# Optimization experiments

Measured on AMD Instinct MI355X. Metric: run time of the kernel, lower is better.

The kernel has to match this reference:

```python
import jax, jax.numpy as jnp
import numpy as np

B, N, CPTS = 16, 4096, 64
M, K, RADIUS = 1024, 32, 0.2
MLP = [64, 64, 128]
EPS = 1e-5  # torch BatchNorm2d default


def setup_inputs() -> dict:
    key = jax.random.key(0)
    ks = jax.random.split(key, 2 + len(MLP))
    inp = {
        "xyz": jax.random.uniform(ks[0], (B, N, 3), dtype=jnp.float32),
        "points": jax.random.normal(ks[1], (B, N, CPTS), dtype=jnp.float32),
    }
    cin = 3 + CPTS
    for i, cout in enumerate(MLP):
        inp[f"W{i}"] = jax.random.normal(ks[2 + i], (cout, cin), dtype=jnp.float32) / np.sqrt(cin)
        inp[f"g{i}"] = jnp.ones((cout,), jnp.float32)
        inp[f"b{i}"] = jnp.zeros((cout,), jnp.float32)
        cin = cout
    return inp


def fps(xyz, m):
    # Farthest point sampling, deterministic start at index 0. Returns (B, m) int32.
    b, n, _ = xyz.shape

    def step(carry, _):
        min_d, far = carry
        cent = jnp.take_along_axis(xyz, far[:, None, None], axis=1)  # (B,1,3)
        d = jnp.sum((xyz - cent) ** 2, axis=-1)                      # (B,N)
        min_d = jnp.minimum(min_d, d)
        return (min_d, jnp.argmax(min_d, axis=-1).astype(jnp.int32)), far

    init = (jnp.full((b, n), 1e10, xyz.dtype), jnp.zeros((b,), jnp.int32))
    _, inds = jax.lax.scan(step, init, None, length=m)
    return inds.T  # (B, m)


def ball_query(xyz, new_xyz, radius, k):
    # Euclidean distances (B,M,N); indices within radius, first-k, pad with first valid.
    d2 = (jnp.sum(new_xyz ** 2, -1)[:, :, None] + jnp.sum(xyz ** 2, -1)[:, None, :]
          - 2.0 * jnp.einsum('bmc,bnc->bmn', new_xyz, xyz))
    dists = jnp.sqrt(jnp.maximum(d2, 0.0))
    n = xyz.shape[1]
    idx = jnp.where(dists > radius, n, jnp.arange(n, dtype=jnp.int32)[None, None, :])
    idx = jnp.sort(idx, axis=-1)[:, :, :k]          # first k in-radius indices (N-padded)
    first = idx[:, :, :1]                           # centroid itself (dist 0) always valid
    return jnp.where(idx == n, first, idx)          # (B, M, k)


def reference(xyz, points, W0, g0, b0, W1, g1, b1, W2, g2, b2):
    bidx = jnp.arange(B)[:, None]
    fps_inds = fps(xyz, M)                          # (B, M)
    new_xyz = xyz[bidx, fps_inds]                   # (B, M, 3)
    g_inds = ball_query(xyz, new_xyz, RADIUS, K)    # (B, M, K)
    bidx2 = jnp.arange(B)[:, None, None]
    grouped_xyz = xyz[bidx2, g_inds] - new_xyz[:, :, None, :]   # (B,M,K,3) local coords
    grouped_pts = points[bidx2, g_inds]                          # (B,M,K,C)
    feats = jnp.concatenate([grouped_xyz, grouped_pts], axis=-1)  # (B,M,K,3+C)

    # 1x1 Conv2d (no bias) + BatchNorm2d (training-mode batch stats) + ReLU
    for Wi, gi, bi in ((W0, g0, b0), (W1, g1, b1), (W2, g2, b2)):
        h = jnp.einsum('bmkc,oc->bmko', feats, Wi)
        mean = h.mean(axis=(0, 1, 2))
        var = h.var(axis=(0, 1, 2))
        feats = jax.nn.relu(gi * (h - mean) * jax.lax.rsqrt(var + EPS) + bi)

    new_points = feats.max(axis=2)                  # max-pool over K -> (B, M, 128)
    return new_xyz, new_points, g_inds
```

## Files before the change

kernel.cpp:

```cpp
#include <hip/hip_runtime.h>
#include <hip/hip_bf16.h>
#include <cstdint>

#define B_ 16
#define N_ 4096
#define CPTS_ 64
#define M_ 1024
#define K_ 32
#define MF_TOT 2097152

using ushort8 = __attribute__((ext_vector_type(8))) unsigned short;
using bf16x8  = __attribute__((ext_vector_type(8))) short;
using f32x4v  = __attribute__((ext_vector_type(4))) float;

static __device__ __forceinline__ unsigned f2bf(float x){
  unsigned u = __float_as_uint(x);
  return (u + 0x7fffu + ((u >> 16) & 1u)) >> 16;
}
static __device__ __forceinline__ float bf2f(unsigned short u){
  return __uint_as_float(((unsigned)u) << 16);
}

#define DPPMAX(v, ctrl)                                                        \
  do {                                                                         \
    int _t = __builtin_amdgcn_update_dpp(0, __float_as_int(v), (ctrl), 0xf,    \
                                         0xf, true);                           \
    (v) = fmaxf((v), __int_as_float(_t));                                      \
  } while (0)

#define STEP(MD, PX, PY, PZ, C, J)                                             \
  { float dx = PX.C - cx, dy = PY.C - cy, dz = PZ.C - cz;                      \
    float d = dx * dx; d = d + dy * dy; d = d + dz * dz;                       \
    float nm = fminf(MD.C, d); MD.C = nm;                                      \
    if (nm > bv){ bv = nm; bj = (J); } }
#define STEP4(MD, PX, PY, PZ, J0)                                              \
  STEP(MD, PX, PY, PZ, x, J0)                                                  \
  STEP(MD, PX, PY, PZ, y, (J0) + 1)                                            \
  STEP(MD, PX, PY, PZ, z, (J0) + 2)                                            \
  STEP(MD, PX, PY, PZ, w, (J0) + 3)

__global__ __launch_bounds__(512, 1) void fps_kernel(const float* __restrict__ xyz,
                                                     float* __restrict__ newxyz){
#pragma clang fp contract(off)
  __shared__ float xs[N_], ys[N_], zs[N_];
  __shared__ int inds_s[M_];
  __shared__ unsigned long long sv_[2][8];
  const int b = blockIdx.x, tid = threadIdx.x;
  const int lane = tid & 63, wv = tid >> 6;
  const float* xb = xyz + (size_t)b * N_ * 3;
  for (int i = tid; i < N_ * 3; i += 512){
    float v = xb[i];
    int n = i / 3, c = i - n * 3;
    if (c == 0) xs[n] = v; else if (c == 1) ys[n] = v; else zs[n] = v;
  }
  __syncthreads();
  const float4 px0 = *reinterpret_cast<const float4*>(&xs[tid * 8 + 0]);
  const float4 px1 = *reinterpret_cast<const float4*>(&xs[tid * 8 + 4]);
  const float4 py0 = *reinterpret_cast<const float4*>(&ys[tid * 8 + 0]);
  const float4 py1 = *reinterpret_cast<const float4*>(&ys[tid * 8 + 4]);
  const float4 pz0 = *reinterpret_cast<const float4*>(&zs[tid * 8 + 0]);
  const float4 pz1 = *reinterpret_cast<const float4*>(&zs[tid * 8 + 4]);
  float4 md0 = make_float4(1e10f, 1e10f, 1e10f, 1e10f);
  float4 md1 = md0;
  int far = 0;
  float cx = xs[0], cy = ys[0], cz = zs[0];
  for (int m = 0; m < M_; ++m){
    if (tid == 0) inds_s[m] = far;
    float bv = -1.0f; int bj = 0;
    STEP4(md0, px0, py0, pz0, 0)
    STEP4(md1, px1, py1, pz1, 4)
    float wm = bv;
    DPPMAX(wm, 0x111);
    DPPMAX(wm, 0x112);
    DPPMAX(wm, 0x114);
    DPPMAX(wm, 0x118);
    DPPMAX(wm, 0x142);
    DPPMAX(wm, 0x143);
    const float wmax = __int_as_float(
        __builtin_amdgcn_readlane(__float_as_int(wm), 63));
    unsigned long long tied = __ballot(bv == wmax);
    const int winlane = (int)__builtin_ctzll(tied);
    const int sl = m & 1;
    if (lane == winlane){
      int wn = tid * 8 + bj;
      sv_[sl][wv] = ((unsigned long long)__float_as_uint(wmax) << 32)
                  | (unsigned)(4095 - wn);
    }
    __syncthreads();
    unsigned long long p0 = sv_[sl][0], p1 = sv_[sl][1], p2 = sv_[sl][2], p3 = sv_[sl][3];
    unsigned long long p4 = sv_[sl][4], p5 = sv_[sl][5], p6 = sv_[sl][6], p7 = sv_[sl][7];
    if (p1 > p0) p0 = p1;
    if (p3 > p2) p2 = p3;
    if (p5 > p4) p4 = p5;
    if (p7 > p6) p6 = p7;
    if (p2 > p0) p0 = p2;
    if (p6 > p4) p4 = p6;
    if (p4 > p0) p0 = p4;
    far = 4095 - (int)(p0 & 0xffffffffu);
    cx = xs[far]; cy = ys[far]; cz = zs[far];
  }
  __syncthreads();
  for (int t = tid; t < M_; t += 512){
    int id = inds_s[t];
    size_t o = ((size_t)b * M_ + t) * 3;
    newxyz[o] = xs[id]; newxyz[o + 1] = ys[id]; newxyz[o + 2] = zs[id];
  }
}

__global__ __launch_bounds__(256) void phi_kernel(const float* __restrict__ xyz,
                                                  const float* __restrict__ points,
                                                  const float* __restrict__ W,
                                                  float* __restrict__ phi){
  __shared__ __align__(16) float Wt[67][64];
  __shared__ __align__(16) float ft[67][128];
  const int tid = threadIdx.x, blk = blockIdx.x;
  const int p0 = blk * 128;
  for (int i = tid; i < 67 * 64; i += 256){
    int o = i / 67, c = i - o * 67;
    Wt[c][o] = W[i];
  }
  const int sl = tid >> 1, half = tid & 1;
  const int p = p0 + sl;
  const float* ps = points + (size_t)p * CPTS_ + half * 32;
  #pragma unroll
  for (int j = 0; j < 8; ++j){
    float4 v = *reinterpret_cast<const float4*>(ps + j * 4);
    int c = 3 + half * 32 + j * 4;
    ft[c][sl] = v.x; ft[c + 1][sl] = v.y; ft[c + 2][sl] = v.z; ft[c + 3][sl] = v.w;
  }
  if (half == 0){
    const float* xp = xyz + (size_t)p * 3;
    ft[0][sl] = xp[0]; ft[1][sl] = xp[1]; ft[2][sl] = xp[2];
  }
  __syncthreads();
  const int sg = tid & 31, og = tid >> 5;
  float acc[4][8];
  #pragma unroll
  for (int i = 0; i < 4; ++i)
    #pragma unroll
    for (int o = 0; o < 8; ++o) acc[i][o] = 0.0f;
  #pragma unroll 2
  for (int c = 0; c < 67; ++c){
    float4 f = *reinterpret_cast<const float4*>(&ft[c][sg * 4]);
    float4 w0 = *reinterpret_cast<const float4*>(&Wt[c][og * 8]);
    float4 w1 = *reinterpret_cast<const float4*>(&Wt[c][og * 8 + 4]);
    const float fv[4] = {f.x, f.y, f.z, f.w};
    #pragma unroll
    for (int i = 0; i < 4; ++i){
      acc[i][0] += fv[i] * w0.x; acc[i][1] += fv[i] * w0.y;
      acc[i][2] += fv[i] * w0.z; acc[i][3] += fv[i] * w0.w;
      acc[i][4] += fv[i] * w1.x; acc[i][5] += fv[i] * w1.y;
      acc[i][6] += fv[i] * w1.z; acc[i][7] += fv[i] * w1.w;
    }
  }
  #pragma unroll
  for (int i = 0; i < 4; ++i){
    float* dst = phi + (size_t)(p0 + sg * 4 + i) * 64 + og * 8;
    *reinterpret_cast<float4*>(dst)     = make_float4(acc[i][0], acc[i][1], acc[i][2], acc[i][3]);
    *reinterpret_cast<float4*>(dst + 4) = make_float4(acc[i][4], acc[i][5], acc[i][6], acc[i][7]);
  }
}

__global__ __launch_bounds__(256) void ballq_psi_kernel(const float* __restrict__ xyz,
                                                        const float* __restrict__ newxyz,
                                                        int* __restrict__ gi,
                                                        float* __restrict__ gif,
                                                        const float* __restrict__ W0,
                                                        float* __restrict__ psi){
  if (blockIdx.x >= 4096){
    const int mi = (blockIdx.x - 4096) * 256 + threadIdx.x;
    const float x = newxyz[(size_t)mi * 3];
    const float y = newxyz[(size_t)mi * 3 + 1];
    const float z = newxyz[(size_t)mi * 3 + 2];
    float* dst = psi + (size_t)mi * 64;
    #pragma unroll
    for (int o4 = 0; o4 < 16; ++o4){
      float v[4];
      #pragma unroll
      for (int e = 0; e < 4; ++e){
        int o = o4 * 4 + e;
        v[e] = fmaf(z, W0[o * 67 + 2], fmaf(y, W0[o * 67 + 1], x * W0[o * 67]));
      }
      *reinterpret_cast<float4*>(dst + o4 * 4) = make_float4(v[0], v[1], v[2], v[3]);
    }
    return;
  }
  const int gw = (blockIdx.x * 256 + threadIdx.x) >> 6;
  const int lane = threadIdx.x & 63;
  const int b = gw >> 10, m = gw & 1023;
  const float* xb = xyz + (size_t)b * N_ * 3;
  const size_t no = (size_t)b * M_ + m;
  const float cx = newxyz[no * 3], cy = newxyz[no * 3 + 1], cz = newxyz[no * 3 + 2];
  const float sm = fmaf(cz, cz, fmaf(cy, cy, cx * cx));
  int total = 0, first_idx = 0; bool havef = false;
  int*   gd = gi  + no * K_;
  float* fd = gif + no * K_;
  for (int ch = 0; ch < 64 && total < K_; ++ch){
    const int n = ch * 64 + lane;
    const float x = xb[n * 3], y = xb[n * 3 + 1], z = xb[n * 3 + 2];
    const float sn = fmaf(z, z, fmaf(y, y, x * x));
    const float dt = fmaf(z, cz, fmaf(y, cy, x * cx));
    float d2 = (sm + sn) - 2.0f * dt;
    float dist = sqrtf(fmaxf(d2, 0.0f));
    bool pred = !(dist > 0.2f);
    unsigned long long mask = __ballot(pred);
    if (!havef && mask){ havef = true; first_idx = ch * 64 + (int)__builtin_ctzll(mask); }
    if (pred){
      int rank = total + (int)__popcll(mask & ((1ull << lane) - 1ull));
      if (rank < K_){ gd[rank] = n; fd[rank] = (float)n; }
    }
    total += (int)__popcll(mask);
  }
  if (total < K_ && lane >= total && lane < K_){ gd[lane] = first_idx; fd[lane] = (float)first_idx; }
}

__global__ __launch_bounds__(256) void stats0_kernel(const float* __restrict__ phi,
                                                     const float* __restrict__ psi,
                                                     const int* __restrict__ gi,
                                                     float* __restrict__ part){
  __shared__ int gidx[128];
  __shared__ float psm[4][64];
  const int tid = threadIdx.x, blk = blockIdx.x;
  const size_t s0 = (size_t)blk * 128;
  const int b  = (int)(s0 >> 15);
  const int m0 = ((int)(s0 & 32767)) >> 5;
  if (tid < 128) gidx[tid] = gi[(size_t)b * 32768 + (size_t)m0 * K_ + tid];
  psm[tid >> 6][tid & 63] =
      psi[((size_t)b * M_ + m0 + (tid >> 6)) * 64 + (tid & 63)];
  __syncthreads();
  const int sg = tid & 31, og = tid >> 5;
  const int mi = sg >> 3;
  float sv[8], sq[8];
  #pragma unroll
  for (int o = 0; o < 8; ++o){ sv[o] = 0.f; sq[o] = 0.f; }
  #pragma unroll
  for (int i = 0; i < 4; ++i){
    const int g = gidx[sg * 4 + i];
    const float* gp = phi + ((size_t)b * N_ + g) * 64 + og * 8;
    float4 a0 = *reinterpret_cast<const float4*>(gp);
    float4 a1 = *reinterpret_cast<const float4*>(gp + 4);
    const float pv[8] = {a0.x, a0.y, a0.z, a0.w, a1.x, a1.y, a1.z, a1.w};
    #pragma unroll
    for (int o = 0; o < 8; ++o){
      float v = pv[o] - psm[mi][og * 8 + o];
      sv[o] += v; sq[o] += v * v;
    }
  }
  #pragma unroll
  for (int off = 1; off < 32; off <<= 1){
    #pragma unroll
    for (int o = 0; o < 8; ++o){
      sv[o] += __shfl_xor(sv[o], off);
      sq[o] += __shfl_xor(sq[o], off);
    }
  }
  if (sg == 0){
    #pragma unroll
    for (int o = 0; o < 8; ++o){
      int ch = og * 8 + o;
      part[(size_t)(ch * 2) * 4096 + blk]     = sv[o];
      part[(size_t)(ch * 2 + 1) * 4096 + blk] = sq[o];
    }
  }
}

template<int CIN, int COUT>
__global__ __launch_bounds__(256) void mlp1_pass(
    const float* __restrict__ phi, const float* __restrict__ psi,
    const int* __restrict__ gi, const float* __restrict__ bnin,
    const float* __restrict__ W,
    unsigned short* __restrict__ hout, float* __restrict__ part)
{
  constexpr int OPT = COUT / 8;
  __shared__ __align__(16) float Wt[CIN][COUT];
  __shared__ __align__(16) float ft[CIN][128];
  const int tid = threadIdx.x, blk = blockIdx.x;
  const size_t s0 = (size_t)blk * 128;

  for (int i = tid; i < CIN * COUT; i += 256){
    int o = i / CIN, c = i - o * CIN;
    Wt[c][o] = W[i];
  }
  {
    __shared__ int gidx[128];
    __shared__ float psm[4][64];
    const int b  = (int)(s0 >> 15);
    const int m0 = ((int)(s0 & 32767)) >> 5;
    if (tid < 128) gidx[tid] = gi[(size_t)b * 32768 + (size_t)m0 * K_ + tid];
    psm[tid >> 6][tid & 63] =
        psi[((size_t)b * M_ + m0 + (tid >> 6)) * 64 + (tid & 63)];
    __syncthreads();
    const int sl = tid >> 1, half = tid & 1;
    const int g = gidx[sl];
    const int mi = sl >> 5;
    const float* gp = phi + ((size_t)b * N_ + g) * 64 + half * 32;
    #pragma unroll
    for (int j = 0; j < 8; ++j){
      float4 v = *reinterpret_cast<const float4*>(gp + j * 4);
      int c = half * 32 + j * 4;
      ft[c][sl]     = fmaxf((v.x - psm[mi][c])     * bnin[c]     + bnin[CIN + c],     0.0f);
      ft[c + 1][sl] = fmaxf((v.y - psm[mi][c + 1]) * bnin[c + 1] + bnin[CIN + c + 1], 0.0f);
      ft[c + 2][sl] = fmaxf((v.z - psm[mi][c + 2]) * bnin[c + 2] + bnin[CIN + c + 2], 0.0f);
      ft[c + 3][sl] = fmaxf((v.w - psm[mi][c + 3]) * bnin[c + 3] + bnin[CIN + c + 3], 0.0f);
    }
  }
  __syncthreads();

  const int sg = tid & 31, og = tid >> 5;
  float acc[4][OPT];
  #pragma unroll
  for (int i = 0; i < 4; ++i)
    #pragma unroll
    for (int o = 0; o < OPT; ++o) acc[i][o] = 0.0f;

  #pragma unroll 2
  for (int c = 0; c < CIN; ++c){
    float4 f = *reinterpret_cast<const float4*>(&ft[c][sg * 4]);
    float4 w[OPT / 4];
    #pragma unroll
    for (int j = 0; j < OPT / 4; ++j)
      w[j] = *reinterpret_cast<const float4*>(&Wt[c][og * OPT + j * 4]);
    const float fv[4] = {f.x, f.y, f.z, f.w};
    #pragma unroll
    for (int i = 0; i < 4; ++i){
      #pragma unroll
      for (int j = 0; j < OPT / 4; ++j){
        acc[i][j * 4 + 0] += fv[i] * w[j].x;
        acc[i][j * 4 + 1] += fv[i] * w[j].y;
        acc[i][j * 4 + 2] += fv[i] * w[j].z;
        acc[i][j * 4 + 3] += fv[i] * w[j].w;
      }
    }
  }

  #pragma unroll
  for (int i = 0; i < 4; ++i){
    size_t s = s0 + sg * 4 + i;
    unsigned pk[OPT / 2];
    #pragma unroll
    for (int o = 0; o < OPT / 2; ++o)
      pk[o] = f2bf(acc[i][2 * o]) | (f2bf(acc[i][2 * o + 1]) << 16);
    uint4* dst = reinterpret_cast<uint4*>(hout + s * COUT + og * OPT);
    dst[0] = make_uint4(pk[0], pk[1], pk[2], pk[3]);
  }
  float sv[OPT], sq[OPT];
  #pragma unroll
  for (int o = 0; o < OPT; ++o){
    float a0 = acc[0][o], a1 = acc[1][o], a2 = acc[2][o], a3 = acc[3][o];
    sv[o] = ((a0 + a1) + a2) + a3;
    sq[o] = ((a0 * a0 + a1 * a1) + a2 * a2) + a3 * a3;
  }
  #pragma unroll
  for (int off = 1; off < 32; off <<= 1){
    #pragma unroll
    for (int o = 0; o < OPT; ++o){
      sv[o] += __shfl_xor(sv[o], off);
      sq[o] += __shfl_xor(sq[o], off);
    }
  }
  if (sg == 0){
    #pragma unroll
    for (int o = 0; o < OPT; ++o){
      int ch = og * OPT + o;
      part[(size_t)(ch * 2) * 4096 + blk]     = sv[o];
      part[(size_t)(ch * 2 + 1) * 4096 + blk] = sq[o];
    }
  }
}

__global__ __launch_bounds__(256) void mlp2_mfma(
    const unsigned short* __restrict__ h1, const float* __restrict__ bn1,
    const float* __restrict__ W2, float* __restrict__ part,
    float* __restrict__ mxmn)
{
  __shared__ unsigned short wsh[128 * 72], wsl[128 * 72];
  __shared__ unsigned short fsh[128 * 72], fsl[128 * 72];
  const int tid = threadIdx.x, blk = blockIdx.x;
  const size_t s0 = (size_t)blk * 128;

  for (int i = tid; i < 128 * 64; i += 256){
    int o = i >> 6, c = i & 63;
    float f = W2[i];
    unsigned hb = f2bf(f);
    float res = f - bf2f((unsigned short)hb);
    wsh[o * 72 + c] = (unsigned short)hb;
    wsl[o * 72 + c] = (unsigned short)f2bf(res);
  }
  {
    const int sl = tid >> 1, c0 = (tid & 1) * 32;
    const unsigned short* hp = h1 + (s0 + sl) * 64 + c0;
    #pragma unroll
    for (int j = 0; j < 4; ++j){
      ushort8 raw = *reinterpret_cast<const ushort8*>(hp + j * 8);
      ushort8 ph, pl;
      #pragma unroll
      for (int e = 0; e < 8; ++e){
        int c = c0 + j * 8 + e;
        float f = fmaxf(bf2f(raw[e]) * bn1[c] + bn1[64 + c], 0.0f);
        unsigned hb = f2bf(f);
        float res = f - bf2f((unsigned short)hb);
        ph[e] = (unsigned short)hb;
        pl[e] = (unsigned short)f2bf(res);
      }
      *reinterpret_cast<ushort8*>(&fsh[sl * 72 + c0 + j * 8]) = ph;
      *reinterpret_cast<ushort8*>(&fsl[sl * 72 + c0 + j * 8]) = pl;
    }
  }
  __syncthreads();

  const int l = tid & 63, w = tid >> 6;
  const int col = l & 15, g = l >> 4;

  bf16x8 bh[2][2], bl[2][2];
  #pragma unroll
  for (int ot = 0; ot < 2; ++ot)
    #pragma unroll
    for (int ks = 0; ks < 2; ++ks){
      int a = (w * 32 + ot * 16 + col) * 72 + ks * 32 + g * 8;
      bh[ot][ks] = *reinterpret_cast<const bf16x8*>(&wsh[a]);
      bl[ot][ks] = *reinterpret_cast<const bf16x8*>(&wsl[a]);
    }

  f32x4v acc[8][2];
  #pragma unroll
  for (int st = 0; st < 8; ++st)
    #pragma unroll
    for (int ot = 0; ot < 2; ++ot)
      acc[st][ot] = (f32x4v){0.f, 0.f, 0.f, 0.f};

  #pragma unroll
  for (int st = 0; st < 8; ++st){
    bf16x8 ah[2], al[2];
    #pragma unroll
    for (int ks = 0; ks < 2; ++ks){
      int a = (st * 16 + col) * 72 + ks * 32 + g * 8;
      ah[ks] = *reinterpret_cast<const bf16x8*>(&fsh[a]);
      al[ks] = *reinterpret_cast<const bf16x8*>(&fsl[a]);
    }
    #pragma unroll
    for (int ot = 0; ot < 2; ++ot){
      #pragma unroll
      for (int ks = 0; ks < 2; ++ks){
        acc[st][ot] = __builtin_amdgcn_mfma_f32_16x16x32_bf16(ah[ks], bh[ot][ks], acc[st][ot], 0, 0, 0);
        acc[st][ot] = __builtin_amdgcn_mfma_f32_16x16x32_bf16(ah[ks], bl[ot][ks], acc[st][ot], 0, 0, 0);
        acc[st][ot] = __builtin_amdgcn_mfma_f32_16x16x32_bf16(al[ks], bh[ot][ks], acc[st][ot], 0, 0, 0);
      }
    }
  }

  #pragma unroll
  for (int ot = 0; ot < 2; ++ot){
    const int ch = w * 32 + ot * 16 + col;
    float sv = 0.f, sq = 0.f;
    float mxm[4], mnm[4];
    #pragma unroll
    for (int j = 0; j < 4; ++j){ mxm[j] = -1e30f; mnm[j] = 1e30f; }
    #pragma unroll
    for (int st = 0; st < 8; ++st){
      f32x4v a = acc[st][ot];
      float t0 = a[0], t1 = a[1], t2 = a[2], t3 = a[3];
      sv += ((t0 + t1) + t2) + t3;
      sq += ((t0 * t0 + t1 * t1) + t2 * t2) + t3 * t3;
      float tmx = fmaxf(fmaxf(t0, t1), fmaxf(t2, t3));
      float tmn = fminf(fminf(t0, t1), fminf(t2, t3));
      mxm[st >> 1] = fmaxf(mxm[st >> 1], tmx);
      mnm[st >> 1] = fminf(mnm[st >> 1], tmn);
    }
    sv += __shfl_xor(sv, 16); sv += __shfl_xor(sv, 32);
    sq += __shfl_xor(sq, 16); sq += __shfl_xor(sq, 32);
    #pragma unroll
    for (int j = 0; j < 4; ++j){
      mxm[j] = fmaxf(mxm[j], __shfl_xor(mxm[j], 16));
      mxm[j] = fmaxf(mxm[j], __shfl_xor(mxm[j], 32));
      mnm[j] = fminf(mnm[j], __shfl_xor(mnm[j], 16));
      mnm[j] = fminf(mnm[j], __shfl_xor(mnm[j], 32));
    }
    if (g == 0){
      part[(size_t)(ch * 2) * 4096 + blk]     = sv;
      part[(size_t)(ch * 2 + 1) * 4096 + blk] = sq;
      #pragma unroll
      for (int j = 0; j < 4; ++j){
        size_t mf = (s0 >> 5) + j;
        mxmn[mf * 128 + ch]          = mxm[j];
        mxmn[MF_TOT + mf * 128 + ch] = mnm[j];
      }
    }
  }
}

__global__ __launch_bounds__(256) void reduce_stats(const float* __restrict__ part,
                                                    const float* __restrict__ g,
                                                    const float* __restrict__ bb,
                                                    float* __restrict__ bn, int cout){
  const int ch = blockIdx.x, tid = threadIdx.x;
  float s = 0.f, q = 0.f;
  const float* ps = part + (size_t)(ch * 2) * 4096;
  const float* pq = part + (size_t)(ch * 2 + 1) * 4096;
  for (int i = tid; i < 4096; i += 256){ s += ps[i]; q += pq[i]; }
  #pragma unroll
  for (int off = 1; off < 64; off <<= 1){ s += __shfl_xor(s, off); q += __shfl_xor(q, off); }
  __shared__ float as_[4], aq_[4];
  if ((tid & 63) == 0){ as_[tid >> 6] = s; aq_[tid >> 6] = q; }
  __syncthreads();
  if (tid == 0){
    float S = as_[0] + as_[1] + as_[2] + as_[3];
    float Q = aq_[0] + aq_[1] + aq_[2] + aq_[3];
    const float cnt = 524288.0f;
    float mean = S / cnt;
    float var  = Q / cnt - mean * mean;
    float sc = g[ch] / sqrtf(var + 1e-5f);
    bn[ch] = sc;
    bn[cout + ch] = bb[ch] - mean * sc;
  }
}

__global__ __launch_bounds__(256) void bn_minmax_finish(const float* __restrict__ mxmn,
                                                        const float* __restrict__ bn2,
                                                        float* __restrict__ out){
  const int i = blockIdx.x * 256 + threadIdx.x;
  const int ch = i & 127;
  const float a = bn2[ch], sh = bn2[128 + ch];
  const float mx = mxmn[i], mn = mxmn[MF_TOT + i];
  out[i] = fmaxf(fmaxf(mx * a + sh, mn * a + sh), 0.0f);
}

extern "C" void kernel_launch(void* const* d_in, const int* in_sizes, int n_in,
                              void* d_out, int out_size, void* d_ws, size_t ws_size,
                              hipStream_t stream){
  (void)in_sizes; (void)n_in; (void)out_size; (void)ws_size;
  const float* xyz    = (const float*)d_in[0];
  const float* points = (const float*)d_in[1];
  const float* W0 = (const float*)d_in[2];
  const float* g0 = (const float*)d_in[3];
  const float* b0 = (const float*)d_in[4];
  const float* W1 = (const float*)d_in[5];
  const float* g1 = (const float*)d_in[6];
  const float* b1 = (const float*)d_in[7];
  const float* W2 = (const float*)d_in[8];
  const float* g2 = (const float*)d_in[9];
  const float* b2 = (const float*)d_in[10];

  float* out = (float*)d_out;
  float* o_newxyz = out;
  float* o_newpts = out + (size_t)B_ * M_ * 3;
  float* o_gind   = out + (size_t)B_ * M_ * 3 + (size_t)B_ * M_ * 128;

  char* ws = (char*)d_ws;
  int*   gi   = (int*)(ws + 0);
  float* part = (float*)(ws + (2ull << 20));
  float* bn0  = (float*)(ws + (6ull << 20));
  float* bn1  = (float*)(ws + (6ull << 20) + 1024);
  float* bn2  = (float*)(ws + (6ull << 20) + 2048);
  float* phi  = (float*)(ws + (8ull << 20));
  float* psi  = (float*)(ws + (24ull << 20));
  unsigned short* h1 = (unsigned short*)(ws + (28ull << 20));
  float* mxmn = (float*)(ws + (92ull << 20));

  phi_kernel<<<512, 256, 0, stream>>>(xyz, points, W0, phi);
  fps_kernel<<<16, 512, 0, stream>>>(xyz, o_newxyz);
  ballq_psi_kernel<<<4160, 256, 0, stream>>>(xyz, o_newxyz, gi, o_gind, W0, psi);

  stats0_kernel<<<4096, 256, 0, stream>>>(phi, psi, gi, part);
  reduce_stats<<<64, 256, 0, stream>>>(part, g0, b0, bn0, 64);

  mlp1_pass<64, 64><<<4096, 256, 0, stream>>>(phi, psi, gi, bn0, W1, h1, part);
  reduce_stats<<<64, 256, 0, stream>>>(part, g1, b1, bn1, 64);

  mlp2_mfma<<<4096, 256, 0, stream>>>(h1, bn1, W2, part, mxmn);
  reduce_stats<<<128, 256, 0, stream>>>(part, g2, b2, bn2, 128);
  bn_minmax_finish<<<MF_TOT / 256, 256, 0, stream>>>(mxmn, bn2, o_newpts);
}
```

Baseline: 938.0 us.

## Replace scalar FP32 layer-1 GEMM with split-bf16 MFMA kernel

Replaces the templated scalar FMA kernel for the second 1x1 conv layer with an MFMA version, mirroring the existing layer-2 kernel. Weights and gathered, normalized activations are split into bf16 hi/lo pairs in shared memory, and three 16x16x32 bf16 MFMAs per k-step approximate an FP32 product. The goal is to cut the ALU cost of the 64x64 GEMM over 524K samples. In exchange it adds split/convert work, scattered 2-byte output stores instead of 16-byte vector stores, and a small precision change from the three-term bf16 split.

```diff
diff --git a/kernel.cpp b/kernel.cpp
--- a/kernel.cpp
+++ b/kernel.cpp
@@ -264,107 +264,109 @@
   }
 }
 
-template<int CIN, int COUT>
-__global__ __launch_bounds__(256) void mlp1_pass(
+__global__ __launch_bounds__(256) void mlp1_mfma(
     const float* __restrict__ phi, const float* __restrict__ psi,
-    const int* __restrict__ gi, const float* __restrict__ bnin,
-    const float* __restrict__ W,
-    unsigned short* __restrict__ hout, float* __restrict__ part)
+    const int* __restrict__ gi, const float* __restrict__ bn0,
+    const float* __restrict__ W1,
+    unsigned short* __restrict__ h1, float* __restrict__ part)
 {
-  constexpr int OPT = COUT / 8;
-  __shared__ __align__(16) float Wt[CIN][COUT];
-  __shared__ __align__(16) float ft[CIN][128];
+  __shared__ unsigned short wsh[64 * 72], wsl[64 * 72];
+  __shared__ unsigned short fsh[128 * 72], fsl[128 * 72];
+  __shared__ int gidx[128];
+  __shared__ float psm[4][64];
   const int tid = threadIdx.x, blk = blockIdx.x;
   const size_t s0 = (size_t)blk * 128;
-
-  for (int i = tid; i < CIN * COUT; i += 256){
-    int o = i / CIN, c = i - o * CIN;
-    Wt[c][o] = W[i];
-  }
+  const int b  = (int)(s0 >> 15);
+  const int m0 = ((int)(s0 & 32767)) >> 5;
+
+  for (int i = tid; i < 64 * 64; i += 256){
+    int o = i >> 6, c = i & 63;
+    float f = W1[i];
+    unsigned hb = f2bf(f);
+    float res = f - bf2f((unsigned short)hb);
+    wsh[o * 72 + c] = (unsigned short)hb;
+    wsl[o * 72 + c] = (unsigned short)f2bf(res);
+  }
+  if (tid < 128) gidx[tid] = gi[(size_t)b * 32768 + (size_t)m0 * K_ + tid];
+  psm[tid >> 6][tid & 63] =
+      psi[((size_t)b * M_ + m0 + (tid >> 6)) * 64 + (tid & 63)];
+  __syncthreads();
   {
-    __shared__ int gidx[128];
-    __shared__ float psm[4][64];
-    const int b  = (int)(s0 >> 15);
-    const int m0 = ((int)(s0 & 32767)) >> 5;
-    if (tid < 128) gidx[tid] = gi[(size_t)b * 32768 + (size_t)m0 * K_ + tid];
-    psm[tid >> 6][tid & 63] =
-        psi[((size_t)b * M_ + m0 + (tid >> 6)) * 64 + (tid & 63)];
-    __syncthreads();
     const int sl = tid >> 1, half = tid & 1;
     const int g = gidx[sl];
     const int mi = sl >> 5;
     const float* gp = phi + ((size_t)b * N_ + g) * 64 + half * 32;
     #pragma unroll
-    for (int j = 0; j < 8; ++j){
-      float4 v = *reinterpret_cast<const float4*>(gp + j * 4);
-      int c = half * 32 + j * 4;
-      ft[c][sl]     = fmaxf((v.x - psm[mi][c])     * bnin[c]     + bnin[CIN + c],     0.0f);
-      ft[c + 1][sl] = fmaxf((v.y - psm[mi][c + 1]) * bnin[c + 1] + bnin[CIN + c + 1], 0.0f);
-      ft[c + 2][sl] = fmaxf((v.z - psm[mi][c + 2]) * bnin[c + 2] + bnin[CIN + c + 2], 0.0f);
-      ft[c + 3][sl] = fmaxf((v.w - psm[mi][c + 3]) * bnin[c + 3] + bnin[CIN + c + 3], 0.0f);
-    }
-  }
-  __syncthreads();
-
-  const int sg = tid & 31, og = tid >> 5;
-  float acc[4][OPT];
-  #pragma unroll
-  for (int i = 0; i < 4; ++i)
-    #pragma unroll
-    for (int o = 0; o < OPT; ++o) acc[i][o] = 0.0f;
-
-  #pragma unroll 2
-  for (int c = 0; c < CIN; ++c){
-    float4 f = *reinterpret_cast<const float4*>(&ft[c][sg * 4]);
-    float4 w[OPT / 4];
-    #pragma unroll
-    for (int j = 0; j < OPT / 4; ++j)
-      w[j] = *reinterpret_cast<const float4*>(&Wt[c][og * OPT + j * 4]);
-    const float fv[4] = {f.x, f.y, f.z, f.w};
-    #pragma unroll
-    for (int i = 0; i < 4; ++i){
+    for (int jj = 0; jj < 4; ++jj){
+      float4 v0 = *reinterpret_cast<const float4*>(gp + jj * 8);
+      float4 v1 = *reinterpret_cast<const float4*>(gp + jj * 8 + 4);
+      const float vv[8] = {v0.x, v0.y, v0.z, v0.w, v1.x, v1.y, v1.z, v1.w};
+      ushort8 ph, pl;
       #pragma unroll
-      for (int j = 0; j < OPT / 4; ++j){
-        acc[i][j * 4 + 0] += fv[i] * w[j].x;
-        acc[i][j * 4 + 1] += fv[i] * w[j].y;
-        acc[i][j * 4 + 2] += fv[i] * w[j].z;
-        acc[i][j * 4 + 3] += fv[i] * w[j].w;
+      for (int e = 0; e < 8; ++e){
+        int c = half * 32 + jj * 8 + e;
+        float f = fmaxf((vv[e] - psm[mi][c]) * bn0[c] + bn0[64 + c], 0.0f);
+        unsigned hb = f2bf(f);
+        float res = f - bf2f((unsigned short)hb);
+        ph[e] = (unsigned short)hb;
+        pl[e] = (unsigned short)f2bf(res);
       }
-    }
-  }
-
-  #pragma unroll
-  for (int i = 0; i < 4; ++i){
-    size_t s = s0 + sg * 4 + i;
-    unsigned pk[OPT / 2];
-    #pragma unroll
-    for (int o = 0; o < OPT / 2; ++o)
-      pk[o] = f2bf(acc[i][2 * o]) | (f2bf(acc[i][2 * o + 1]) << 16);
-    uint4* dst = reinterpret_cast<uint4*>(hout + s * COUT + og * OPT);
-    dst[0] = make_uint4(pk[0], pk[1], pk[2], pk[3]);
-  }
-  float sv[OPT], sq[OPT];
-  #pragma unroll
-  for (int o = 0; o < OPT; ++o){
-    float a0 = acc[0][o], a1 = acc[1][o], a2 = acc[2][o], a3 = acc[3][o];
-    sv[o] = ((a0 + a1) + a2) + a3;
-    sq[o] = ((a0 * a0 + a1 * a1) + a2 * a2) + a3 * a3;
-  }
-  #pragma unroll
-  for (int off = 1; off < 32; off <<= 1){
-    #pragma unroll
-    for (int o = 0; o < OPT; ++o){
-      sv[o] += __shfl_xor(sv[o], off);
-      sq[o] += __shfl_xor(sq[o], off);
-    }
-  }
-  if (sg == 0){
-    #pragma unroll
-    for (int o = 0; o < OPT; ++o){
-      int ch = og * OPT + o;
-      part[(size_t)(ch * 2) * 4096 + blk]     = sv[o];
-      part[(size_t)(ch * 2 + 1) * 4096 + blk] = sq[o];
-    }
+      *reinterpret_cast<ushort8*>(&fsh[sl * 72 + half * 32 + jj * 8]) = ph;
+      *reinterpret_cast<ushort8*>(&fsl[sl * 72 + half * 32 + jj * 8]) = pl;
+    }
+  }
+  __syncthreads();
+
+  const int l = tid & 63, w = tid >> 6;
+  const int col = l & 15, g4 = l >> 4;
+  const int ch = w * 16 + col;
+
+  bf16x8 bh[2], bl[2];
+  #pragma unroll
+  for (int ks = 0; ks < 2; ++ks){
+    int a = ch * 72 + ks * 32 + g4 * 8;
+    bh[ks] = *reinterpret_cast<const bf16x8*>(&wsh[a]);
+    bl[ks] = *reinterpret_cast<const bf16x8*>(&wsl[a]);
+  }
+
+  f32x4v acc[8];
+  #pragma unroll
+  for (int st = 0; st < 8; ++st) acc[st] = (f32x4v){0.f, 0.f, 0.f, 0.f};
+
+  #pragma unroll
+  for (int st = 0; st < 8; ++st){
+    #pragma unroll
+    for (int ks = 0; ks < 2; ++ks){
+      int a = (st * 16 + col) * 72 + ks * 32 + g4 * 8;
+      bf16x8 ah = *reinterpret_cast<const bf16x8*>(&fsh[a]);
+      bf16x8 al = *reinterpret_cast<const bf16x8*>(&fsl[a]);
+      acc[st] = __builtin_amdgcn_mfma_f32_16x16x32_bf16(ah, bh[ks], acc[st], 0, 0, 0);
+      acc[st] = __builtin_amdgcn_mfma_f32_16x16x32_bf16(ah, bl[ks], acc[st], 0, 0, 0);
+      acc[st] = __builtin_amdgcn_mfma_f32_16x16x32_bf16(al, bh[ks], acc[st], 0, 0, 0);
+    }
+  }
+
+  #pragma unroll
+  for (int st = 0; st < 8; ++st){
+    size_t sbase = s0 + st * 16 + g4 * 4;
+    #pragma unroll
+    for (int r = 0; r < 4; ++r)
+      h1[(sbase + r) * 64 + ch] = (unsigned short)f2bf(acc[st][r]);
+  }
+
+  float sv = 0.f, sq = 0.f;
+  #pragma unroll
+  for (int st = 0; st < 8; ++st){
+    f32x4v a = acc[st];
+    float t0 = a[0], t1 = a[1], t2 = a[2], t3 = a[3];
+    sv += ((t0 + t1) + t2) + t3;
+    sq += ((t0 * t0 + t1 * t1) + t2 * t2) + t3 * t3;
+  }
+  sv += __shfl_xor(sv, 16); sv += __shfl_xor(sv, 32);
+  sq += __shfl_xor(sq, 16); sq += __shfl_xor(sq, 32);
+  if (g4 == 0){
+    part[(size_t)(ch * 2) * 4096 + blk]     = sv;
+    part[(size_t)(ch * 2 + 1) * 4096 + blk] = sq;
   }
 }
 
@@ -563,7 +565,7 @@
   stats0_kernel<<<4096, 256, 0, stream>>>(phi, psi, gi, part);
   reduce_stats<<<64, 256, 0, stream>>>(part, g0, b0, bn0, 64);
 
-  mlp1_pass<64, 64><<<4096, 256, 0, stream>>>(phi, psi, gi, bn0, W1, h1, part);
+  mlp1_mfma<<<4096, 256, 0, stream>>>(phi, psi, gi, bn0, W1, h1, part);
   reduce_stats<<<64, 256, 0, stream>>>(part, g1, b1, bn1, 64);
 
   mlp2_mfma<<<4096, 256, 0, stream>>>(h1, bn1, W2, part, mxmn);
```

Measured after the change: 905.1 us. -3.5%, faster.
